# Performance work log

Hardware: AMD Instinct MI355X
Metric: run time of the kernel (lower is better)

Reference implementation:

```python
import jax, jax.numpy as jnp
import numpy as np

B, T, C = 2, 2048, 4096
NH, NKV, HD = 32, 8, 128
GROUPS = NH // NKV
THETA = 10000.0


def _rope_tables(seq_len, dim, theta, dtype):
    inv_freq = 1.0 / (theta ** (jnp.arange(0, dim, 2, dtype=jnp.float32) / dim))
    t = jnp.arange(seq_len, dtype=jnp.float32)
    freqs = jnp.outer(t, inv_freq)            # [T, dim/2]
    emb = jnp.concatenate([freqs, freqs], -1)  # [T, dim]
    return jnp.cos(emb).astype(dtype), jnp.sin(emb).astype(dtype)


def _rotate_half(x):
    h = x.shape[-1] // 2
    return jnp.concatenate([-x[..., h:], x[..., :h]], axis=-1)


def setup_inputs() -> dict:
    key = jax.random.key(0)
    ks = jax.random.split(key, 5)
    s = 1.0 / np.sqrt(C)
    return {
        "x": jax.random.normal(ks[0], (B, T, C), jnp.float32),
        "wq": jax.random.normal(ks[1], (C, NH * HD), jnp.float32) * s,
        "wk": jax.random.normal(ks[2], (C, NKV * HD), jnp.float32) * s,
        "wv": jax.random.normal(ks[3], (C, NKV * HD), jnp.float32) * s,
        "wo": jax.random.normal(ks[4], (NH * HD, C), jnp.float32) * s,
    }


def reference(x, wq, wk, wv, wo):
    b, t, c = x.shape
    q = (x @ wq).reshape(b, t, NH, HD).transpose(0, 2, 1, 3)    # [B,NH,T,HD]
    k = (x @ wk).reshape(b, t, NKV, HD).transpose(0, 2, 1, 3)   # [B,NKV,T,HD]
    v = (x @ wv).reshape(b, t, NKV, HD).transpose(0, 2, 1, 3)
    cos, sin = _rope_tables(t, HD, THETA, x.dtype)              # [T,HD]
    cos = cos[None, None]
    sin = sin[None, None]
    q = q * cos + _rotate_half(q) * sin
    k = k * cos + _rotate_half(k) * sin
    # GQA: broadcast KV heads over groups via einsum instead of materializing repeat
    qg = q.reshape(b, NKV, GROUPS, t, HD)
    scores = jnp.einsum('bkgqd,bkld->bkgql', qg, k) * (HD ** -0.5)  # [B,NKV,G,T,T]
    causal = jnp.triu(jnp.full((t, t), -jnp.inf, dtype=x.dtype), k=1)
    scores = scores + causal
    attn = jax.nn.softmax(scores, axis=-1)
    out = jnp.einsum('bkgql,bkld->bkgqd', attn, v)              # [B,NKV,G,T,HD]
    out = out.reshape(b, NH, t, HD).transpose(0, 2, 1, 3).reshape(b, t, NH * HD)
    return out @ wo
```

## Files before the change

### kernel.cpp

```cpp
#include <hip/hip_runtime.h>
#include <hip/hip_bf16.h>
#include <math.h>

#define B_ 2
#define T_ 2048
#define C_ 4096
#define NH_ 32
#define NKV_ 8
#define HD_ 128
#define M_ (B_*T_)
#define QKVN_ (NH_*HD_ + 2*NKV_*HD_)

using bf16 = __hip_bfloat16;
typedef __bf16 bf16x8 __attribute__((ext_vector_type(8)));
typedef float f32x4 __attribute__((ext_vector_type(4)));

__device__ inline f32x4 mfma16(bf16x8 a, bf16x8 b, f32x4 c) {
    return __builtin_amdgcn_mfma_f32_16x16x32_bf16(a, b, c, 0, 0, 0);
}

__global__ __launch_bounds__(256) void cast_f32_bf16(const float* __restrict__ in,
                                                     bf16* __restrict__ out, int n4) {
    int i = blockIdx.x * 256 + threadIdx.x;
    if (i >= n4) return;
    float4 v = reinterpret_cast<const float4*>(in)[i];
    union { bf16 h[4]; uint2 u; } o;
    o.h[0] = __float2bfloat16(v.x);
    o.h[1] = __float2bfloat16(v.y);
    o.h[2] = __float2bfloat16(v.z);
    o.h[3] = __float2bfloat16(v.w);
    reinterpret_cast<uint2*>(out)[i] = o.u;
}

__global__ __launch_bounds__(256) void transpose_cast(const float* __restrict__ in,
                                                      bf16* __restrict__ out, int K, int N) {
    __shared__ float tile[32][33];
    int tx = threadIdx.x & 31, ty = threadIdx.x >> 5;
    int n0 = blockIdx.x << 5, k0 = blockIdx.y << 5;
#pragma unroll
    for (int p = 0; p < 4; ++p)
        tile[p*8 + ty][tx] = in[(size_t)(k0 + p*8 + ty) * N + n0 + tx];
    __syncthreads();
#pragma unroll
    for (int p = 0; p < 4; ++p)
        out[(size_t)(n0 + p*8 + ty) * K + k0 + tx] = __float2bfloat16(tile[tx][p*8 + ty]);
}

__device__ inline void store_out(float* p, float v) { *p = v; }
__device__ inline void store_out(bf16*  p, float v) { *p = __float2bfloat16(v); }

template <typename OutT>
__global__ __launch_bounds__(512, 2) void gemm256(const bf16* __restrict__ A,
                                                  const bf16* __restrict__ Bt,
                                                  OutT* __restrict__ C,
                                                  int M, int N, int K) {
    __shared__ __align__(16) char lds[131072];
    const int tid = threadIdx.x;
    const int wid = tid >> 6, lane = tid & 63;
    const int lq = lane & 15, lg = lane >> 4;
    const int wrow = wid >> 2, wcol = wid & 3;

    const int nwg = gridDim.x;
    const int q8 = nwg >> 3;
    const int wg = (blockIdx.x & 7) * q8 + (blockIdx.x >> 3);
    const int nby = M >> 8;
    const int by = wg % nby, bx = wg / nby;
    const int brow = by << 8, bcol = bx << 8;

    const bf16* Ag = A + (size_t)brow * K;
    const bf16* Bg = Bt + (size_t)bcol * K;
    const int nt = K >> 6;

    const int srow = (wid << 3) + (lane >> 3);
    const int schunk = (lane & 7) ^ ((lane >> 3) & 7);

#define STAGE_HALF(gbase, ldsoff, t2, cbuf, hf)                                         \
    {                                                                                   \
        _Pragma("unroll")                                                               \
        for (int l = 0; l < 2; ++l) {                                                   \
            const int r0 = (hf) * 128 + l * 64;                                         \
            const char* src = (const char*)(gbase) +                                    \
                ((size_t)(r0 + srow) * K + (size_t)(t2) * 64) * 2 + schunk * 16;        \
            char* dst = &lds[(ldsoff) + (cbuf) * 32768 + (r0 + (wid << 3)) * 128];      \
            __builtin_amdgcn_global_load_lds(                                           \
                (const __attribute__((address_space(1))) void*)src,                     \
                (__attribute__((address_space(3))) void*)dst, 16, 0, 0);                \
        }                                                                               \
    }

#define LDA(cbuf, mh, mf, ks) \
    (*(const bf16x8*)&lds[(cbuf)*32768 + (wrow*128 + (mh)*64 + (mf)*16 + lq)*128 + ((((ks)*4 + lg)) ^ (lq & 7))*16])
#define LDB(cbuf, nh, nf, ks) \
    (*(const bf16x8*)&lds[65536 + (cbuf)*32768 + (wcol*64 + (nh)*32 + (nf)*16 + lq)*128 + ((((ks)*4 + lg)) ^ (lq & 7))*16])

#define READ_A(cbuf, mh) \
    { _Pragma("unroll") for (int mf = 0; mf < 4; ++mf) { a[mf][0] = LDA(cbuf, mh, mf, 0); a[mf][1] = LDA(cbuf, mh, mf, 1); } }
#define READ_B(cbuf, nh, breg) \
    { _Pragma("unroll") for (int nf = 0; nf < 2; ++nf) { breg[nf][0] = LDB(cbuf, nh, nf, 0); breg[nf][1] = LDB(cbuf, nh, nf, 1); } }
#define MFMA_Q(am, an, breg)                                                     \
    { __builtin_amdgcn_s_setprio(1);                                             \
      _Pragma("unroll") for (int mf = 0; mf < 4; ++mf)                           \
          _Pragma("unroll") for (int nf = 0; nf < 2; ++nf)                       \
              _Pragma("unroll") for (int ks = 0; ks < 2; ++ks)                   \
                  acc[(am) + mf][(an) + nf] = mfma16(a[mf][ks], breg[nf][ks],    \
                                                     acc[(am) + mf][(an) + nf]); \
      __builtin_amdgcn_s_setprio(0); }
#define BAR() __builtin_amdgcn_s_barrier()

    f32x4 acc[8][4] = {};
    bf16x8 a[4][2], b0[2][2], b1[2][2];

    STAGE_HALF(Ag, 0,     0, 0, 0); STAGE_HALF(Ag, 0,     0, 0, 1);
    STAGE_HALF(Bg, 65536, 0, 0, 0); STAGE_HALF(Bg, 65536, 0, 0, 1);
    STAGE_HALF(Bg, 65536, 1, 1, 0); STAGE_HALF(Bg, 65536, 1, 1, 1);
    asm volatile("s_waitcnt vmcnt(4)" ::: "memory");
    BAR();

    for (int i = 0; i < (nt >> 1); ++i) {
        const int u = 2 * i;
        const bool s_u2 = (u + 2) < nt;
        const bool s_v2 = (u + 3) < nt;

        READ_A(0, 0); READ_B(0, 0, b0);
        STAGE_HALF(Ag, 0, u + 1, 1, 0);
        MFMA_Q(0, 0, b0);
        BAR();
        READ_B(0, 1, b1);
        STAGE_HALF(Ag, 0, u + 1, 1, 1);
        MFMA_Q(0, 2, b1);
        BAR();
        READ_A(0, 1);
        if (s_u2) STAGE_HALF(Bg, 65536, u + 2, 0, 0);
        MFMA_Q(4, 2, b1);
        BAR();
        if (s_u2) STAGE_HALF(Bg, 65536, u + 2, 0, 1);
        MFMA_Q(4, 0, b0);
        if (s_u2) asm volatile("s_waitcnt vmcnt(4)" ::: "memory");
        else      asm volatile("s_waitcnt vmcnt(0)" ::: "memory");
        BAR();
        READ_A(1, 0); READ_B(1, 0, b0);
        if (s_u2) STAGE_HALF(Ag, 0, u + 2, 0, 0);
        MFMA_Q(0, 0, b0);
        BAR();
        READ_B(1, 1, b1);
        if (s_u2) STAGE_HALF(Ag, 0, u + 2, 0, 1);
        MFMA_Q(0, 2, b1);
        BAR();
        READ_A(1, 1);
        if (s_v2) STAGE_HALF(Bg, 65536, u + 3, 1, 0);
        MFMA_Q(4, 2, b1);
        BAR();
        if (s_v2) STAGE_HALF(Bg, 65536, u + 3, 1, 1);
        MFMA_Q(4, 0, b0);
        if (s_v2) asm volatile("s_waitcnt vmcnt(4)" ::: "memory");
        else      asm volatile("s_waitcnt vmcnt(0)" ::: "memory");
        BAR();
    }
#undef STAGE_HALF
#undef LDA
#undef LDB
#undef READ_A
#undef READ_B
#undef MFMA_Q
#undef BAR

#pragma unroll
    for (int mf = 0; mf < 8; ++mf)
#pragma unroll
        for (int nf = 0; nf < 4; ++nf)
#pragma unroll
            for (int r = 0; r < 4; ++r) {
                int row = brow + wrow * 128 + mf * 16 + lg * 4 + r;
                int col = bcol + wcol * 64 + nf * 16 + lq;
                store_out(&C[(size_t)row * N + col], acc[mf][nf][r]);
            }
}

__global__ __launch_bounds__(256) void rope_qk(const bf16* __restrict__ qkv,
                                               bf16* __restrict__ outp,
                                               int nheads, int col_off, float qscale) {
    size_t idx = (size_t)blockIdx.x * 256 + threadIdx.x;
    int i = (int)(idx & 63);
    size_t rest = idx >> 6;
    int t = (int)(rest % T_);
    rest /= T_;
    int hh = (int)(rest % nheads);
    int b = (int)(rest / nheads);

    const bf16* src = qkv + (size_t)(b * T_ + t) * QKVN_ + col_off + hh * HD_;
    float x0 = __bfloat162float(src[i]);
    float x1 = __bfloat162float(src[i + 64]);
    float inv = exp2f((float)i * -0.20762050593045952f);
    float th = (float)t * inv;
    float s = sinf(th), c = cosf(th);
    bf16* dst = outp + ((size_t)(b * nheads + hh) * T_ + t) * HD_;
    dst[i]      = __float2bfloat16((x0 * c - x1 * s) * qscale);
    dst[i + 64] = __float2bfloat16((x1 * c + x0 * s) * qscale);
}

__global__ __launch_bounds__(256) void vtrans(const bf16* __restrict__ qkv,
                                              bf16* __restrict__ vt) {
    __shared__ bf16 tile[32][33];
    int gx = blockIdx.x;
    int dt = gx & 3;
    int tt = (gx >> 2) & 63;
    int kv = (gx >> 8) & 7;
    int b  = gx >> 11;
    int d0 = dt * 32, t0 = tt * 32;
    int tx = threadIdx.x & 31, ty = threadIdx.x >> 5;

    const bf16* src = qkv + (size_t)(b * T_ + t0) * QKVN_ + (NH_*HD_ + NKV_*HD_) + kv * HD_ + d0;
#pragma unroll
    for (int p = 0; p < 4; ++p)
        tile[p*8 + ty][tx] = src[(size_t)(p*8 + ty) * QKVN_ + tx];
    __syncthreads();
    bf16* dst = vt + ((size_t)((b * NKV_ + kv) * HD_ + d0)) * T_ + t0;
#pragma unroll
    for (int p = 0; p < 4; ++p)
        dst[(size_t)(p*8 + ty) * T_ + tx] = tile[tx][p*8 + ty];
}

__global__ __launch_bounds__(512) void fattn(const bf16* __restrict__ Q,
                                             const bf16* __restrict__ Kt,
                                             const bf16* __restrict__ VT,
                                             bf16* __restrict__ O) {
    const int lin = blockIdx.x;
    const int kv = lin & 7;
    const int b  = (lin >> 3) & 1;
    const int idx = lin >> 4;
    const int h  = kv * 4 + (idx & 3);
    const int jp = idx >> 2;

    const int tid = threadIdx.x, wid = tid >> 6, lane = tid & 63;
    const int lq = lane & 15, lg = lane >> 4;

    const bf16* Kp = Kt + (size_t)(b * NKV_ + kv) * T_ * HD_;
    const bf16* Vp = VT + (size_t)(b * NKV_ + kv) * HD_ * T_;

    __shared__ __align__(16) bf16 Ks[2][64][128];
    __shared__ __align__(16) bf16 Vs[2][128][64];
    __shared__ __align__(16) bf16 p_lds[8][32][72];

    const float THR_L2 = 11.5416f;

#define STAGE_KV(cbuf, tt)                                                           \
    { _Pragma("unroll") for (int j = 0; j < 2; ++j) {                                \
        int kidx = j * 64 + lane;                                                    \
        int krow = wid * 8 + (kidx >> 4);                                            \
        int kch  = (kidx & 15) ^ (krow & 15);                                        \
        const bf16* ksrc = Kp + (size_t)((tt) * 64 + krow) * HD_ + kch * 8;          \
        __builtin_amdgcn_global_load_lds(                                            \
            (const __attribute__((address_space(1))) void*)ksrc,                     \
            (__attribute__((address_space(3))) void*)&Ks[cbuf][wid*8 + j*4][0],      \
            16, 0, 0);                                                               \
      }                                                                              \
      _Pragma("unroll") for (int j = 0; j < 2; ++j) {                                \
        int vidx = j * 64 + lane;                                                    \
        int vrow = wid * 16 + (vidx >> 3);                                           \
        int vch  = (vidx & 7) ^ (vrow & 7);                                          \
        const bf16* vsrc = Vp + (size_t)vrow * T_ + (tt) * 64 + vch * 8;             \
        __builtin_amdgcn_global_load_lds(                                            \
            (const __attribute__((address_space(1))) void*)vsrc,                     \
            (__attribute__((address_space(3))) void*)&Vs[cbuf][wid*16 + j*8][0],     \
            16, 0, 0);                                                               \
      } }

    for (int half = 0; half < 2; ++half) {
        const int qt = half ? (7 - jp) : jp;
        const int q0 = qt * 256 + wid * 32;
        const int kv_end = q0 + 32;
        const int NT = qt * 4 + 4;

        const bf16* Qp = Q + ((size_t)(b * NH_ + h) * T_ + q0) * HD_;
        bf16x8 qf[2][4];
#pragma unroll
        for (int m = 0; m < 2; ++m)
#pragma unroll
            for (int c = 0; c < 4; ++c)
                qf[m][c] = *(const bf16x8*)&Qp[(size_t)(m*16 + lq) * HD_ + c * 32 + lg * 8];

        f32x4 oacc[2][8] = {};
        float m_r[2] = {-INFINITY, -INFINITY};
        float l_r[2] = {0.f, 0.f};

        STAGE_KV(0, 0);
        STAGE_KV(1, 1);
        asm volatile("s_waitcnt vmcnt(4)" ::: "memory");
        __builtin_amdgcn_s_barrier();

        for (int t = 0; t < NT; ++t) {
            const int cb = t & 1;
            const int t0 = t * 64;

            if (t0 < kv_end) {
                f32x4 st[2][4] = {};
#pragma unroll
                for (int n = 0; n < 4; ++n) {
                    bf16x8 kf[4];
#pragma unroll
                    for (int c = 0; c < 4; ++c)
                        kf[c] = *(const bf16x8*)((const char*)&Ks[cb][n*16 + lq][0]
                                                  + (((c*4 + lg) ^ lq) << 4));
                    __builtin_amdgcn_s_setprio(1);
#pragma unroll
                    for (int c = 0; c < 4; ++c) {
                        st[0][n] = mfma16(kf[c], qf[0][c], st[0][n]);
                        st[1][n] = mfma16(kf[c], qf[1][c], st[1][n]);
                    }
                    __builtin_amdgcn_s_setprio(0);
                }

#pragma unroll
                for (int m = 0; m < 2; ++m) {
                    const int qq = q0 + m*16 + lq;
#pragma unroll
                    for (int n = 0; n < 4; ++n)
#pragma unroll
                        for (int r = 0; r < 4; ++r) {
                            int kk = t0 + n*16 + lg*4 + r;
                            if (kk > qq) st[m][n][r] = -INFINITY;
                        }
                }

                float rmax[2];
#pragma unroll
                for (int m = 0; m < 2; ++m) {
                    float v = st[m][0][0];
#pragma unroll
                    for (int n = 0; n < 4; ++n)
#pragma unroll
                        for (int r = 0; r < 4; ++r) v = fmaxf(v, st[m][n][r]);
                    v = fmaxf(v, __shfl_xor(v, 16));
                    v = fmaxf(v, __shfl_xor(v, 32));
                    rmax[m] = v;
                }

                float dmax = fmaxf(rmax[0] - m_r[0], rmax[1] - m_r[1]);
                if (__any(dmax > THR_L2)) {
#pragma unroll
                    for (int m = 0; m < 2; ++m) {
                        float mnew = fmaxf(m_r[m], rmax[m]);
                        float alpha = exp2f(m_r[m] - mnew);
                        m_r[m] = mnew;
                        l_r[m] *= alpha;
#pragma unroll
                        for (int r = 0; r < 4; ++r) {
                            float a_pv = __shfl(alpha, lg*4 + r);
#pragma unroll
                            for (int f = 0; f < 8; ++f) oacc[m][f][r] *= a_pv;
                        }
                    }
                }

#pragma unroll
                for (int m = 0; m < 2; ++m) {
                    float rsum = 0.f;
#pragma unroll
                    for (int n = 0; n < 4; ++n)
#pragma unroll
                        for (int r = 0; r < 4; ++r) {
                            float p = exp2f(st[m][n][r] - m_r[m]);
                            st[m][n][r] = p;
                            rsum += p;
                        }
                    rsum += __shfl_xor(rsum, 16);
                    rsum += __shfl_xor(rsum, 32);
                    l_r[m] += rsum;
                }

#pragma unroll
                for (int m = 0; m < 2; ++m)
#pragma unroll
                    for (int n = 0; n < 4; ++n) {
                        union { bf16 hh[4]; uint2 u; } pk;
#pragma unroll
                        for (int r = 0; r < 4; ++r) pk.hh[r] = __float2bfloat16(st[m][n][r]);
                        *(uint2*)&p_lds[wid][m*16 + lq][n*16 + lg*4] = pk.u;
                    }

#pragma unroll
                for (int ks = 0; ks < 2; ++ks) {
                    bf16x8 pa0 = *(const bf16x8*)&p_lds[wid][lq]     [ks*32 + lg*8];
                    bf16x8 pa1 = *(const bf16x8*)&p_lds[wid][16 + lq][ks*32 + lg*8];
                    bf16x8 vf[8];
#pragma unroll
                    for (int f = 0; f < 8; ++f)
                        vf[f] = *(const bf16x8*)((const char*)&Vs[cb][f*16 + lq][0]
                                                  + (((ks*4 + lg) ^ (lq & 7)) << 4));
                    __builtin_amdgcn_s_setprio(1);
#pragma unroll
                    for (int f = 0; f < 8; ++f) {
                        oacc[0][f] = mfma16(pa0, vf[f], oacc[0][f]);
                        oacc[1][f] = mfma16(pa1, vf[f], oacc[1][f]);
                    }
                    __builtin_amdgcn_s_setprio(0);
                }
            }

            __builtin_amdgcn_s_barrier();
            if (t + 2 < NT) {
                STAGE_KV(cb, t + 2);
                asm volatile("s_waitcnt vmcnt(4)" ::: "memory");
            } else {
                asm volatile("s_waitcnt vmcnt(0)" ::: "memory");
            }
            __builtin_amdgcn_s_barrier();
        }

#pragma unroll
        for (int m = 0; m < 2; ++m) {
            float rinv = __builtin_amdgcn_rcpf(l_r[m]);
#pragma unroll
            for (int r = 0; r < 4; ++r) {
                float rl = __shfl(rinv, lg*4 + r);
                int row = q0 + m*16 + lg*4 + r;
#pragma unroll
                for (int f = 0; f < 8; ++f) {
                    int d = f*16 + lq;
                    O[((size_t)(b * T_ + row) * NH_ + h) * HD_ + d] =
                        __float2bfloat16(oacc[m][f][r] * rl);
                }
            }
        }
    }
#undef STAGE_KV
}

extern "C" void kernel_launch(void* const* d_in, const int* in_sizes, int n_in,
                              void* d_out, int out_size, void* d_ws, size_t ws_size,
                              hipStream_t stream) {
    const float* x  = (const float*)d_in[0];
    const float* wq = (const float*)d_in[1];
    const float* wk = (const float*)d_in[2];
    const float* wv = (const float*)d_in[3];
    const float* wo = (const float*)d_in[4];
    float* out = (float*)d_out;

    bf16* ws    = (bf16*)d_ws;
    bf16* xb    = ws;
    bf16* wqkvT = xb + (size_t)M_ * C_;
    bf16* woT   = wqkvT + (size_t)QKVN_ * C_;
    bf16* qkv   = woT + (size_t)C_ * C_;

    bf16* attn = xb;
    bf16* q_r  = wqkvT;
    bf16* k_r  = q_r + (size_t)B_ * NH_ * T_ * HD_;
    bf16* vt   = k_r + (size_t)B_ * NKV_ * T_ * HD_;

    cast_f32_bf16<<<(M_ * C_ / 4 + 255) / 256, 256, 0, stream>>>(x, xb, M_ * C_ / 4);
    transpose_cast<<<dim3(128, 128), 256, 0, stream>>>(wq, wqkvT, C_, NH_ * HD_);
    transpose_cast<<<dim3(32, 128), 256, 0, stream>>>(wk, wqkvT + (size_t)(NH_ * HD_) * C_, C_, NKV_ * HD_);
    transpose_cast<<<dim3(32, 128), 256, 0, stream>>>(wv, wqkvT + (size_t)(NH_ * HD_ + NKV_ * HD_) * C_, C_, NKV_ * HD_);
    transpose_cast<<<dim3(128, 128), 256, 0, stream>>>(wo, woT, NH_ * HD_, C_);

    gemm256<bf16><<<dim3((QKVN_ / 256) * (M_ / 256)), 512, 0, stream>>>(xb, wqkvT, qkv, M_, QKVN_, C_);

    rope_qk<<<(B_ * NH_ * T_ * 64) / 256, 256, 0, stream>>>(qkv, q_r, NH_, 0, 0.12751741230963214f);
    rope_qk<<<(B_ * NKV_ * T_ * 64) / 256, 256, 0, stream>>>(qkv, k_r, NKV_, NH_ * HD_, 1.0f);
    vtrans<<<B_ * NKV_ * (T_ / 32) * (HD_ / 32), 256, 0, stream>>>(qkv, vt);

    fattn<<<dim3(256), 512, 0, stream>>>(q_r, k_r, vt, attn);

    gemm256<float><<<dim3((C_ / 256) * (M_ / 256)), 512, 0, stream>>>(attn, woT, out, M_, C_, C_);
}
```

Before: 527.0 us.

## Use 16 waves per attention block with 16 query rows per wave

After: 521.7 us. About the same (-1.0%).

```diff
diff --git a/kernel.cpp b/kernel.cpp
--- a/kernel.cpp
+++ b/kernel.cpp
@@ -220,10 +220,10 @@
         dst[(size_t)(p*8 + ty) * T_ + tx] = tile[tx][p*8 + ty];
 }
 
-__global__ __launch_bounds__(512) void fattn(const bf16* __restrict__ Q,
-                                             const bf16* __restrict__ Kt,
-                                             const bf16* __restrict__ VT,
-                                             bf16* __restrict__ O) {
+__global__ __launch_bounds__(1024) void fattn(const bf16* __restrict__ Q,
+                                              const bf16* __restrict__ Kt,
+                                              const bf16* __restrict__ VT,
+                                              bf16* __restrict__ O) {
     const int lin = blockIdx.x;
     const int kv = lin & 7;
     const int b  = (lin >> 3) & 1;
@@ -239,53 +239,49 @@
 
     __shared__ __align__(16) bf16 Ks[2][64][128];
     __shared__ __align__(16) bf16 Vs[2][128][64];
-    __shared__ __align__(16) bf16 p_lds[8][32][72];
+    __shared__ __align__(16) bf16 p_lds[16][16][72];
 
     const float THR_L2 = 11.5416f;
 
 #define STAGE_KV(cbuf, tt)                                                           \
-    { _Pragma("unroll") for (int j = 0; j < 2; ++j) {                                \
-        int kidx = j * 64 + lane;                                                    \
-        int krow = wid * 8 + (kidx >> 4);                                            \
-        int kch  = (kidx & 15) ^ (krow & 15);                                        \
+    { {                                                                              \
+        int krow = wid * 4 + (lane >> 4);                                            \
+        int kch  = (lane & 15) ^ (krow & 15);                                        \
         const bf16* ksrc = Kp + (size_t)((tt) * 64 + krow) * HD_ + kch * 8;          \
         __builtin_amdgcn_global_load_lds(                                            \
             (const __attribute__((address_space(1))) void*)ksrc,                     \
-            (__attribute__((address_space(3))) void*)&Ks[cbuf][wid*8 + j*4][0],      \
+            (__attribute__((address_space(3))) void*)&Ks[cbuf][wid*4][0],            \
             16, 0, 0);                                                               \
       }                                                                              \
-      _Pragma("unroll") for (int j = 0; j < 2; ++j) {                                \
-        int vidx = j * 64 + lane;                                                    \
-        int vrow = wid * 16 + (vidx >> 3);                                           \
-        int vch  = (vidx & 7) ^ (vrow & 7);                                          \
+      {                                                                              \
+        int vrow = wid * 8 + (lane >> 3);                                            \
+        int vch  = (lane & 7) ^ (vrow & 7);                                          \
         const bf16* vsrc = Vp + (size_t)vrow * T_ + (tt) * 64 + vch * 8;             \
         __builtin_amdgcn_global_load_lds(                                            \
             (const __attribute__((address_space(1))) void*)vsrc,                     \
-            (__attribute__((address_space(3))) void*)&Vs[cbuf][wid*16 + j*8][0],     \
+            (__attribute__((address_space(3))) void*)&Vs[cbuf][wid*8][0],            \
             16, 0, 0);                                                               \
       } }
 
     for (int half = 0; half < 2; ++half) {
         const int qt = half ? (7 - jp) : jp;
-        const int q0 = qt * 256 + wid * 32;
-        const int kv_end = q0 + 32;
+        const int q0 = qt * 256 + wid * 16;
+        const int kv_end = q0 + 16;
         const int NT = qt * 4 + 4;
 
         const bf16* Qp = Q + ((size_t)(b * NH_ + h) * T_ + q0) * HD_;
-        bf16x8 qf[2][4];
-#pragma unroll
-        for (int m = 0; m < 2; ++m)
-#pragma unroll
-            for (int c = 0; c < 4; ++c)
-                qf[m][c] = *(const bf16x8*)&Qp[(size_t)(m*16 + lq) * HD_ + c * 32 + lg * 8];
-
-        f32x4 oacc[2][8] = {};
-        float m_r[2] = {-INFINITY, -INFINITY};
-        float l_r[2] = {0.f, 0.f};
+        bf16x8 qf[4];
+#pragma unroll
+        for (int c = 0; c < 4; ++c)
+            qf[c] = *(const bf16x8*)&Qp[(size_t)lq * HD_ + c * 32 + lg * 8];
+
+        f32x4 oacc[8] = {};
+        float m_r = -INFINITY;
+        float l_r = 0.f;
 
         STAGE_KV(0, 0);
         STAGE_KV(1, 1);
-        asm volatile("s_waitcnt vmcnt(4)" ::: "memory");
+        asm volatile("s_waitcnt vmcnt(2)" ::: "memory");
         __builtin_amdgcn_s_barrier();
 
         for (int t = 0; t < NT; ++t) {
@@ -293,7 +289,7 @@
             const int t0 = t * 64;
 
             if (t0 < kv_end) {
-                f32x4 st[2][4] = {};
+                f32x4 st[4] = {};
 #pragma unroll
                 for (int n = 0; n < 4; ++n) {
                     bf16x8 kf[4];
@@ -303,85 +299,65 @@
                                                   + (((c*4 + lg) ^ lq) << 4));
                     __builtin_amdgcn_s_setprio(1);
 #pragma unroll
-                    for (int c = 0; c < 4; ++c) {
-                        st[0][n] = mfma16(kf[c], qf[0][c], st[0][n]);
-                        st[1][n] = mfma16(kf[c], qf[1][c], st[1][n]);
-                    }
+                    for (int c = 0; c < 4; ++c)
+                        st[n] = mfma16(kf[c], qf[c], st[n]);
                     __builtin_amdgcn_s_setprio(0);
                 }
 
-#pragma unroll
-                for (int m = 0; m < 2; ++m) {
-                    const int qq = q0 + m*16 + lq;
-#pragma unroll
-                    for (int n = 0; n < 4; ++n)
-#pragma unroll
-                        for (int r = 0; r < 4; ++r) {
-                            int kk = t0 + n*16 + lg*4 + r;
-                            if (kk > qq) st[m][n][r] = -INFINITY;
-                        }
-                }
-
-                float rmax[2];
-#pragma unroll
-                for (int m = 0; m < 2; ++m) {
-                    float v = st[m][0][0];
-#pragma unroll
-                    for (int n = 0; n < 4; ++n)
-#pragma unroll
-                        for (int r = 0; r < 4; ++r) v = fmaxf(v, st[m][n][r]);
-                    v = fmaxf(v, __shfl_xor(v, 16));
-                    v = fmaxf(v, __shfl_xor(v, 32));
-                    rmax[m] = v;
-                }
-
-                float dmax = fmaxf(rmax[0] - m_r[0], rmax[1] - m_r[1]);
-                if (__any(dmax > THR_L2)) {
-#pragma unroll
-                    for (int m = 0; m < 2; ++m) {
-                        float mnew = fmaxf(m_r[m], rmax[m]);
-                        float alpha = exp2f(m_r[m] - mnew);
-                        m_r[m] = mnew;
-                        l_r[m] *= alpha;
-#pragma unroll
-                        for (int r = 0; r < 4; ++r) {
-                            float a_pv = __shfl(alpha, lg*4 + r);
-#pragma unroll
-                            for (int f = 0; f < 8; ++f) oacc[m][f][r] *= a_pv;
-                        }
+                const int qq = q0 + lq;
+#pragma unroll
+                for (int n = 0; n < 4; ++n)
+#pragma unroll
+                    for (int r = 0; r < 4; ++r) {
+                        int kk = t0 + n*16 + lg*4 + r;
+                        if (kk > qq) st[n][r] = -INFINITY;
+                    }
+
+                float rmax = st[0][0];
+#pragma unroll
+                for (int n = 0; n < 4; ++n)
+#pragma unroll
+                    for (int r = 0; r < 4; ++r) rmax = fmaxf(rmax, st[n][r]);
+                rmax = fmaxf(rmax, __shfl_xor(rmax, 16));
+                rmax = fmaxf(rmax, __shfl_xor(rmax, 32));
+
+                if (__any(rmax - m_r > THR_L2)) {
+                    float mnew = fmaxf(m_r, rmax);
+                    float alpha = exp2f(m_r - mnew);
+                    m_r = mnew;
+                    l_r *= alpha;
+#pragma unroll
+                    for (int r = 0; r < 4; ++r) {
+                        float a_pv = __shfl(alpha, lg*4 + r);
+#pragma unroll
+                        for (int f = 0; f < 8; ++f) oacc[f][r] *= a_pv;
                     }
                 }
 
-#pragma unroll
-                for (int m = 0; m < 2; ++m) {
-                    float rsum = 0.f;
-#pragma unroll
-                    for (int n = 0; n < 4; ++n)
-#pragma unroll
-                        for (int r = 0; r < 4; ++r) {
-                            float p = exp2f(st[m][n][r] - m_r[m]);
-                            st[m][n][r] = p;
-                            rsum += p;
-                        }
-                    rsum += __shfl_xor(rsum, 16);
-                    rsum += __shfl_xor(rsum, 32);
-                    l_r[m] += rsum;
+                float rsum = 0.f;
+#pragma unroll
+                for (int n = 0; n < 4; ++n)
+#pragma unroll
+                    for (int r = 0; r < 4; ++r) {
+                        float p = exp2f(st[n][r] - m_r);
+                        st[n][r] = p;
+                        rsum += p;
+                    }
+                rsum += __shfl_xor(rsum, 16);
+                rsum += __shfl_xor(rsum, 32);
+                l_r += rsum;
+
+#pragma unroll
+                for (int n = 0; n < 4; ++n) {
+                    union { bf16 hh[4]; uint2 u; } pk;
+#pragma unroll
+                    for (int r = 0; r < 4; ++r) pk.hh[r] = __float2bfloat16(st[n][r]);
+                    *(uint2*)&p_lds[wid][lq][n*16 + lg*4] = pk.u;
                 }
 
 #pragma unroll
-                for (int m = 0; m < 2; ++m)
-#pragma unroll
-                    for (int n = 0; n < 4; ++n) {
-                        union { bf16 hh[4]; uint2 u; } pk;
-#pragma unroll
-                        for (int r = 0; r < 4; ++r) pk.hh[r] = __float2bfloat16(st[m][n][r]);
-                        *(uint2*)&p_lds[wid][m*16 + lq][n*16 + lg*4] = pk.u;
-                    }
-
-#pragma unroll
                 for (int ks = 0; ks < 2; ++ks) {
-                    bf16x8 pa0 = *(const bf16x8*)&p_lds[wid][lq]     [ks*32 + lg*8];
-                    bf16x8 pa1 = *(const bf16x8*)&p_lds[wid][16 + lq][ks*32 + lg*8];
+                    bf16x8 pa = *(const bf16x8*)&p_lds[wid][lq][ks*32 + lg*8];
                     bf16x8 vf[8];
 #pragma unroll
                     for (int f = 0; f < 8; ++f)
@@ -389,10 +365,8 @@
                                                   + (((ks*4 + lg) ^ (lq & 7)) << 4));
                     __builtin_amdgcn_s_setprio(1);
 #pragma unroll
-                    for (int f = 0; f < 8; ++f) {
-                        oacc[0][f] = mfma16(pa0, vf[f], oacc[0][f]);
-                        oacc[1][f] = mfma16(pa1, vf[f], oacc[1][f]);
-                    }
+                    for (int f = 0; f < 8; ++f)
+                        oacc[f] = mfma16(pa, vf[f], oacc[f]);
                     __builtin_amdgcn_s_setprio(0);
                 }
             }
@@ -400,25 +374,24 @@
             __builtin_amdgcn_s_barrier();
             if (t + 2 < NT) {
                 STAGE_KV(cb, t + 2);
-                asm volatile("s_waitcnt vmcnt(4)" ::: "memory");
+                asm volatile("s_waitcnt vmcnt(2)" ::: "memory");
             } else {
                 asm volatile("s_waitcnt vmcnt(0)" ::: "memory");
             }
             __builtin_amdgcn_s_barrier();
         }
 
-#pragma unroll
-        for (int m = 0; m < 2; ++m) {
-            float rinv = __builtin_amdgcn_rcpf(l_r[m]);
+        {
+            float rinv = __builtin_amdgcn_rcpf(l_r);
 #pragma unroll
             for (int r = 0; r < 4; ++r) {
                 float rl = __shfl(rinv, lg*4 + r);
-                int row = q0 + m*16 + lg*4 + r;
+                int row = q0 + lg*4 + r;
 #pragma unroll
                 for (int f = 0; f < 8; ++f) {
                     int d = f*16 + lq;
                     O[((size_t)(b * T_ + row) * NH_ + h) * HD_ + d] =
-                        __float2bfloat16(oacc[m][f][r] * rl);
+                        __float2bfloat16(oacc[f][r] * rl);
                 }
             }
         }
@@ -459,7 +432,7 @@
     rope_qk<<<(B_ * NKV_ * T_ * 64) / 256, 256, 0, stream>>>(qkv, k_r, NKV_, NH_ * HD_, 1.0f);
     vtrans<<<B_ * NKV_ * (T_ / 32) * (HD_ / 32), 256, 0, stream>>>(qkv, vt);
 
-    fattn<<<dim3(256), 512, 0, stream>>>(q_r, k_r, vt, attn);
+    fattn<<<dim3(256), 1024, 0, stream>>>(q_r, k_r, vt, attn);
 
     gemm256<float><<<dim3((C_ / 256) * (M_ / 256)), 512, 0, stream>>>(attn, woT, out, M_, C_, C_);
 }
```
